# Kernel optimization log

Hardware: AMD Instinct MI355X
Metric: run time of the kernel (lower is better)

Reference implementation:

```python
import jax, jax.numpy as jnp
import numpy as np

MAX_SEQ, D, VOCAB, N_LAYERS = 2048, 256, 240, 6
DH = 64.0  # scale used inside RelativeGlobalAttention
BATCH = 4


def _pos_embedding():
    # sin(pow(pos*1e-5, i/D) - pi/2 * ((i+1)%2)), exactly as in __init__
    pos = np.arange(MAX_SEQ, dtype=np.float64)[:, None]
    i = np.arange(D, dtype=np.float64)[None, :]
    ang = np.power(pos * 1e-5, i / D) - np.pi * 0.5 * ((i + 1) % 2)
    return jnp.asarray(np.sin(ang), dtype=jnp.float32)  # [L, D]


def _skew(QE):
    # pad a zero column in front, reshape [B,L,L+1]->[B,L+1,L], drop first row
    B, L, _ = QE.shape
    cat = jnp.concatenate([jnp.zeros((B, L, 1), QE.dtype), QE], axis=2)
    return cat.reshape(B, L + 1, L)[:, 1:, :]


def _rel_attn(x, Wq, Wk, Wv):
    Q = x @ Wq  # [B,L,D]
    K = x @ Wk
    V = x @ Wv
    QE = jnp.einsum('bld,bmd->blm', Q, K - Q)      # Q @ (K-Q)^T
    Srel = _skew(QE)
    QKt = jnp.einsum('bld,bmd->blm', Q, K)
    scores = (QKt + Srel) / jnp.sqrt(jnp.asarray(DH, x.dtype))
    probs = jax.nn.softmax(scores, axis=-1)        # no causal mask in source
    return probs @ V


def setup_inputs() -> dict:
    key = jax.random.key(0)
    ks = jax.random.split(key, 16)
    s = 1.0 / np.sqrt(D)
    mk = lambda k, shape, sc: (jax.random.normal(k, shape, jnp.float32) * sc)
    inp = {
        'tokens': jax.random.randint(ks[0], (BATCH, MAX_SEQ), 0, VOCAB),
        'embed_table': mk(ks[1], (VOCAB, D), 0.05),
        'Wq1': mk(ks[2], (N_LAYERS, D, D), s),
        'Wk1': mk(ks[3], (N_LAYERS, D, D), s),
        'Wv1': mk(ks[4], (N_LAYERS, D, D), s),
        'Wq2': mk(ks[5], (N_LAYERS, D, D), s),
        'Wk2': mk(ks[6], (N_LAYERS, D, D), s),
        'Wv2': mk(ks[7], (N_LAYERS, D, D), s),
        'Wf1': mk(ks[8], (N_LAYERS, D, D), s),
        'bf1': jnp.zeros((N_LAYERS, D), jnp.float32),
        'Wf2': mk(ks[9], (N_LAYERS, D, D), s),
        'bf2': jnp.zeros((N_LAYERS, D), jnp.float32),
        'Wfc': mk(ks[10], (MAX_SEQ * D, VOCAB), 1.0 / np.sqrt(MAX_SEQ * D)),
        'bfc': jnp.zeros((VOCAB,), jnp.float32),
    }
    return inp


def reference(tokens, embed_table, Wq1, Wk1, Wv1, Wq2, Wk2, Wv2,
              Wf1, bf1, Wf2, bf2, Wfc, bfc):
    x = embed_table[tokens] + _pos_embedding()[None]  # [B,L,D]
    for i in range(N_LAYERS):
        x = _rel_attn(x, Wq1[i], Wk1[i], Wv1[i]) + x
        x = _rel_attn(x, Wq2[i], Wk2[i], Wv2[i]) + x
        h = jax.nn.leaky_relu(x @ Wf1[i] + bf1[i], negative_slope=0.2)
        x = h @ Wf2[i] + bf2[i]
        # NOTE: BatchNorm layers exist in source but are never called in _decoder
    flat = x.reshape(x.shape[0], -1)  # [B, L*D]
    return jax.nn.softmax(flat @ Wfc + bfc, axis=-1)  # [B, vocab]
```

## Files before the change

### kernel.cpp

```cpp
#include <hip/hip_runtime.h>
#include <hip/hip_fp16.h>

typedef unsigned short u16;
typedef unsigned int   u32;

#define BB 4
#define LL 2048
#define DD 256
#define VV 240
#define NLAYERS 6

static constexpr long BLD = (long)BB * LL * DD;
static constexpr long LD_ = (long)LL * DD;
static constexpr long LxL = (long)LL * LL;
static constexpr long BLL = (long)BB * LxL;

typedef _Float16 h8  __attribute__((ext_vector_type(8)));
typedef float  f32x4 __attribute__((ext_vector_type(4)));

__device__ __forceinline__ u16 f2h(float f) {
    _Float16 h = (_Float16)f;
    return __builtin_bit_cast(u16, h);
}
__device__ __forceinline__ float h2f(u16 u) {
    return (float)__builtin_bit_cast(_Float16, u);
}

__device__ __forceinline__ void gl16(const void* g, void* l) {
    __builtin_amdgcn_global_load_lds((const __attribute__((address_space(1))) void*)g,
                                     (__attribute__((address_space(3))) void*)l, 16, 0, 0);
}

__global__ __launch_bounds__(256)
void embed_kernel(const int* __restrict__ tokens, const float* __restrict__ table,
                  float* __restrict__ x, u16* __restrict__ xh)
{
    long idx = (long)blockIdx.x * 256 + threadIdx.x;
    if (idx >= BLD) return;
    int i  = (int)(idx & (DD - 1));
    long bl = idx >> 8;
    int l  = (int)(bl & (LL - 1));
    int tok = tokens[bl];
    float base = (float)l * 1e-5f;
    float p = powf(base, (float)i * (1.0f / (float)DD));
    float ang = p - ((i & 1) ? 0.0f : 1.57079632679489662f);
    float v = table[(long)tok * DD + i] + sinf(ang);
    x[idx] = v;
    xh[idx] = f2h(v);
}

template<bool DIFF>
__global__ __launch_bounds__(256)
void wconv(const float* __restrict__ W, const float* __restrict__ Wsub,
           u16* __restrict__ Wt, long lstride)
{
    int blk = blockIdx.x;
    int m  = blk >> 6;
    int ti = (blk >> 3) & 7;
    int tj = blk & 7;
    const float* src = W + (long)m * 65536;
    u16* dst = Wt + (long)m * lstride;
    __shared__ float tile[32][33];
    int t = threadIdx.x;
    int c = t & 31, r8 = t >> 5;
    #pragma unroll
    for (int p = 0; p < 4; ++p) {
        int r = r8 + p * 8;
        long off = (long)(ti * 32 + r) * 256 + tj * 32 + c;
        float v = src[off];
        if constexpr (DIFF) v -= Wsub[(long)m * 65536 + off];
        tile[r][c] = v;
    }
    __syncthreads();
    #pragma unroll
    for (int p = 0; p < 4; ++p) {
        int n = r8 + p * 8;
        dst[(long)(tj * 32 + n) * 256 + ti * 32 + c] = f2h(tile[c][n]);
    }
}

template<int EPI, int BM, int BN>
__global__ __launch_bounds__(256)
void gemm_mfma(const u16* __restrict__ A, const u16* __restrict__ B,
               const u16* __restrict__ B2,
               const float* __restrict__ bias, const float* __restrict__ Cres,
               float* __restrict__ Cf, u16* __restrict__ Ch,
               u16* __restrict__ Ch2, u16* __restrict__ Ch3, u16* __restrict__ Ch4,
               int M, int N, int K, int ldA,
               long sA, long sB, long sC)
{
    constexpr int FM = BM / 32, FN = BN / 32;
    __shared__ u16 As[2][BM * 32];
    __shared__ u16 Bs[2][BN * 32];
    const int bz = blockIdx.z;
    A += (long)bz * sA;
    const int bm = blockIdx.y * BM;
    const int bn = blockIdx.x * BN;
    int bnb = bn;
    const u16* Bp;
    if constexpr (EPI & 128) {
        Bp = (bn >= LL) ? B2 : B;
        if (bn >= LL) bnb = bn - LL;
        Bp += (long)bz * sB;
    } else {
        Bp = B + (long)bz * sB;
    }
    if constexpr (EPI & 4)  Cres += (long)bz * sC;
    if constexpr (EPI & 8)  Cf   += (long)bz * sC;
    if constexpr ((EPI & 16) && !(EPI & (64 | 128))) Ch += (long)bz * sC;

    const int t = threadIdx.x;
    const int lane = t & 63, wave = t >> 6;
    const int wm = (wave >> 1) * (BM / 2), wn = (wave & 1) * (BN / 2);

    f32x4 acc[FM][FN];
    #pragma unroll
    for (int i = 0; i < FM; ++i)
        #pragma unroll
        for (int j = 0; j < FN; ++j)
            acc[i][j] = (f32x4){0.f, 0.f, 0.f, 0.f};

    const u16* gA0 = A  + (long)(bm  + (t >> 2)) * ldA + (t & 3) * 8;
    const u16* gB0 = Bp + (long)(bnb + (t >> 2)) * K   + (t & 3) * 8;

    const int arow = wm + (lane & 15);
    const int brow = wn + (lane & 15);
    const int ko = (lane >> 4) * 8;

    #define STAGE(buf, koff) do {                                              \
        gl16(gA0 + (koff), &As[buf][wave * 512]);                              \
        if constexpr (BM == 128) gl16(gA0 + 64L * ldA + (koff),                \
                                      &As[buf][2048 + wave * 512]);            \
        gl16(gB0 + (koff), &Bs[buf][wave * 512]);                              \
        if constexpr (BN == 128) gl16(gB0 + 64L * K + (koff),                  \
                                      &Bs[buf][2048 + wave * 512]);            \
    } while (0)

    STAGE(0, 0);
    int cur = 0;
    for (int k0 = 0; k0 < K; k0 += 32) {
        __syncthreads();
        if (k0 + 32 < K) {
            if (cur) STAGE(0, k0 + 32);
            else     STAGE(1, k0 + 32);
        }
        h8 af[FM], bf[FN];
        #pragma unroll
        for (int i = 0; i < FM; ++i) af[i] = *(const h8*)&As[cur][(arow + i * 16) * 32 + ko];
        #pragma unroll
        for (int j = 0; j < FN; ++j) bf[j] = *(const h8*)&Bs[cur][(brow + j * 16) * 32 + ko];
        #pragma unroll
        for (int i = 0; i < FM; ++i)
            #pragma unroll
            for (int j = 0; j < FN; ++j)
                acc[i][j] = __builtin_amdgcn_mfma_f32_16x16x32_f16(af[i], bf[j], acc[i][j], 0, 0, 0);
        cur ^= 1;
    }
    #undef STAGE

    const int colc = lane & 15;
    const int rowb = (lane >> 4) * 4;
    if constexpr (EPI & 64) {
        const int seg = bn >> 8;
        const int nb  = bn & 255;
        if (seg < 3) {
            u16* dst = (seg == 0) ? Ch : ((seg == 1) ? Ch2 : Ch3);
            #pragma unroll
            for (int i = 0; i < FM; ++i)
                #pragma unroll
                for (int j = 0; j < FN; ++j) {
                    int nn = nb + wn + j * 16 + colc;
                    #pragma unroll
                    for (int r = 0; r < 4; ++r) {
                        long row = bm + wm + i * 16 + rowb + r;
                        dst[row * DD + nn] = f2h(acc[i][j][r]);
                    }
                }
        } else {
            #pragma unroll
            for (int i = 0; i < FM; ++i) {
                int r0 = bm + wm + i * 16 + rowb;
                int b  = r0 >> 11;
                int m0 = r0 & (LL - 1);
                #pragma unroll
                for (int j = 0; j < FN; ++j) {
                    int nn = nb + wn + j * 16 + colc;
                    f32x4 v = acc[i][j];
                    ushort4 pk;
                    pk.x = f2h(v.x); pk.y = f2h(v.y); pk.z = f2h(v.z); pk.w = f2h(v.w);
                    *(ushort4*)&Ch4[((long)b * DD + nn) * LL + m0] = pk;
                }
            }
        }
    } else if constexpr (EPI & 128) {
        u16* dst = ((bn >= LL) ? Ch2 : Ch) + (long)bz * sC;
        const int nb = bn & (LL - 1);
        #pragma unroll
        for (int i = 0; i < FM; ++i)
            #pragma unroll
            for (int j = 0; j < FN; ++j) {
                int n = nb + wn + j * 16 + colc;
                #pragma unroll
                for (int r = 0; r < 4; ++r) {
                    long row = bm + wm + i * 16 + rowb + r;
                    dst[row * LL + n] = f2h(acc[i][j][r]);
                }
            }
    } else {
        #pragma unroll
        for (int i = 0; i < FM; ++i) {
            #pragma unroll
            for (int j = 0; j < FN; ++j) {
                int n = bn + wn + j * 16 + colc;
                float bv = (EPI & 1) ? bias[n] : 0.f;
                #pragma unroll
                for (int r = 0; r < 4; ++r) {
                    long row = bm + wm + i * 16 + rowb + r;
                    float val = acc[i][j][r] + bv;
                    if (EPI & 2) val = (val >= 0.f) ? val : 0.2f * val;
                    long off = row * (long)N + n;
                    if (EPI & 4) val += Cres[off];
                    if (EPI & 8) Cf[off] = val;
                    if (EPI & 16) Ch[off] = f2h(val);
                }
            }
        }
    }
}

__global__ __launch_bounds__(256)
void skew_softmax(u16* __restrict__ S1, const u16* __restrict__ QE)
{
    const int bi = blockIdx.x;
    const int b = bi >> 11;
    const int i = bi & (LL - 1);
    u16* srow = S1 + (long)bi * LL;
    const u16* qe_i  = QE + ((long)b * LL + i) * LL;
    const u16* qe_i1 = qe_i + ((i + 1 < LL) ? LL : 0);
    const int t = threadIdx.x;

    uint4 sv = ((const uint4*)srow)[t];
    const u16* se = (const u16*)&sv;
    float vals[8];
    float mx = -1e30f;
    #pragma unroll
    for (int j = 0; j < 8; ++j) {
        int m = t * 8 + j;
        float srel;
        if (m <= i)            srel = h2f(qe_i[m - i + (LL - 1)]);
        else if (m == i + 1)   srel = 0.f;
        else                   srel = h2f(qe_i1[m - i - 2]);
        float s = (h2f(se[j]) + srel) * 0.125f;
        vals[j] = s;
        mx = fmaxf(mx, s);
    }
    #pragma unroll
    for (int off = 32; off >= 1; off >>= 1)
        mx = fmaxf(mx, __shfl_xor(mx, off, 64));
    __shared__ float redm[4], reds[4];
    const int wid = t >> 6;
    if ((t & 63) == 0) redm[wid] = mx;
    __syncthreads();
    mx = fmaxf(fmaxf(redm[0], redm[1]), fmaxf(redm[2], redm[3]));

    float sum = 0.f;
    #pragma unroll
    for (int j = 0; j < 8; ++j) { vals[j] = expf(vals[j] - mx); sum += vals[j]; }
    #pragma unroll
    for (int off = 32; off >= 1; off >>= 1)
        sum += __shfl_xor(sum, off, 64);
    if ((t & 63) == 0) reds[wid] = sum;
    __syncthreads();
    sum = reds[0] + reds[1] + reds[2] + reds[3];
    float inv = 1.0f / sum;
    uint4 ov;
    u16* oe = (u16*)&ov;
    #pragma unroll
    for (int j = 0; j < 8; ++j) oe[j] = f2h(vals[j] * inv);
    ((uint4*)srow)[t] = ov;
}

__global__ __launch_bounds__(960)
void fc_partial(const float* __restrict__ x, const float* __restrict__ W,
                float* __restrict__ part)
{
    const int v = threadIdx.x;
    const int b = threadIdx.y;
    const int chunk = blockIdx.x;
    const int KC = (int)(LD_ / 256);
    const long k0 = (long)chunk * KC;
    const float* xb = x + (long)b * LD_ + k0;
    const float* Wp = W + k0 * VV + v;
    float acc = 0.f;
    #pragma unroll 4
    for (int k2 = 0; k2 < KC; ++k2)
        acc = fmaf(xb[k2], Wp[(long)k2 * VV], acc);
    part[((long)chunk * BB + b) * VV + v] = acc;
}

__global__ __launch_bounds__(960)
void fc_finish(const float* __restrict__ part, const float* __restrict__ bias,
               float* __restrict__ out)
{
    const int v = threadIdx.x, b = threadIdx.y;
    float acc = bias[v];
    for (int c = 0; c < 256; ++c)
        acc += part[((long)c * BB + b) * VV + v];
    __shared__ float lds[BB][VV];
    __shared__ float mxs[BB], sms[BB];
    lds[b][v] = acc;
    __syncthreads();
    if (v == 0) {
        float m = -1e30f;
        for (int j = 0; j < VV; ++j) m = fmaxf(m, lds[b][j]);
        float s = 0.f;
        for (int j = 0; j < VV; ++j) s += expf(lds[b][j] - m);
        mxs[b] = m; sms[b] = s;
    }
    __syncthreads();
    out[b * VV + v] = expf(lds[b][v] - mxs[b]) / sms[b];
}

extern "C" void kernel_launch(void* const* d_in, const int* in_sizes, int n_in,
                              void* d_out, int out_size, void* d_ws, size_t ws_size,
                              hipStream_t stream)
{
    const int*   tokens = (const int*)d_in[0];
    const float* table  = (const float*)d_in[1];
    const float* Wq1 = (const float*)d_in[2];
    const float* Wk1 = (const float*)d_in[3];
    const float* Wv1 = (const float*)d_in[4];
    const float* Wq2 = (const float*)d_in[5];
    const float* Wk2 = (const float*)d_in[6];
    const float* Wv2 = (const float*)d_in[7];
    const float* Wf1 = (const float*)d_in[8];
    const float* bf1 = (const float*)d_in[9];
    const float* Wf2 = (const float*)d_in[10];
    const float* bf2 = (const float*)d_in[11];
    const float* Wfc = (const float*)d_in[12];
    const float* bfc = (const float*)d_in[13];

    char* p = (char*)d_ws;
    float* x  = (float*)p; p += BLD * 4;
    u16* xh = (u16*)p;     p += BLD * 2;
    u16* qb = (u16*)p;     p += BLD * 2;
    u16* kb = (u16*)p;     p += BLD * 2;
    u16* eb = (u16*)p;     p += BLD * 2;
    u16* vt = (u16*)p;     p += BLD * 2;
    u16* S1 = (u16*)p;     p += BLL * 2;
    u16* QE = (u16*)p;     p += BLL * 2;
    u16* qkevw = (u16*)p;  p += 12L * 4 * 65536 * 2;
    u16* fw = (u16*)p;     p += 12L * 65536 * 2;
    float* part = (float*)p;
    u16* hb = qb;

    const long LS = 4 * 65536;
    wconv<false><<<384, 256, 0, stream>>>(Wq1, nullptr, qkevw + 0L * 65536, LS);
    wconv<false><<<384, 256, 0, stream>>>(Wk1, nullptr, qkevw + 1L * 65536, LS);
    wconv<true ><<<384, 256, 0, stream>>>(Wk1, Wq1,     qkevw + 2L * 65536, LS);
    wconv<false><<<384, 256, 0, stream>>>(Wv1, nullptr, qkevw + 3L * 65536, LS);
    wconv<false><<<384, 256, 0, stream>>>(Wq2, nullptr, qkevw + 24L * 65536, LS);
    wconv<true ><<<384, 256, 0, stream>>>(Wk2, Wq2,     qkevw + 24L * 65536 + 2 * 65536, LS);
    wconv<false><<<384, 256, 0, stream>>>(Wk2, nullptr, qkevw + 24L * 65536 + 1 * 65536, LS);
    wconv<false><<<384, 256, 0, stream>>>(Wv2, nullptr, qkevw + 24L * 65536 + 3 * 65536, LS);
    wconv<false><<<384, 256, 0, stream>>>(Wf1, nullptr, fw, 65536);
    wconv<false><<<384, 256, 0, stream>>>(Wf2, nullptr, fw + 6L * 65536, 65536);

    embed_kernel<<<(int)((BLD + 255) / 256), 256, 0, stream>>>(tokens, table, x, xh);

    const dim3 gqkev(8, 64, 1);
    const dim3 gscore(32, 16, BB);
    const dim3 gpv(4, 32, BB);
    const dim3 gffn(4, 128, 1);

    for (int layer = 0; layer < NLAYERS; ++layer) {
        for (int half = 0; half < 2; ++half) {
            const u16* wqkev = qkevw + ((long)(half * 6 + layer)) * LS;
            gemm_mfma<64, 128, 128><<<gqkev, 256, 0, stream>>>(
                xh, wqkev, nullptr, nullptr, nullptr, nullptr, qb, kb, eb, vt,
                BB * LL, 1024, DD, DD, 0, 0, 0);
            gemm_mfma<128, 128, 128><<<gscore, 256, 0, stream>>>(
                qb, kb, eb, nullptr, nullptr, nullptr, S1, QE, nullptr, nullptr,
                LL, LL, DD, DD, LD_, LD_, LxL);
            skew_softmax<<<BB * LL, 256, 0, stream>>>(S1, QE);
            gemm_mfma<4 | 8 | 16, 64, 64><<<gpv, 256, 0, stream>>>(
                S1, vt, nullptr, nullptr, x, x, xh, nullptr, nullptr, nullptr,
                LL, DD, LL, LL, LxL, LD_, LD_);
        }
        gemm_mfma<1 | 2 | 16, 64, 64><<<gffn, 256, 0, stream>>>(
            xh, fw + (long)layer * 65536, nullptr, bf1 + layer * DD, nullptr,
            nullptr, hb, nullptr, nullptr, nullptr, BB * LL, DD, DD, DD, 0, 0, 0);
        gemm_mfma<1 | 8 | 16, 64, 64><<<gffn, 256, 0, stream>>>(
            hb, fw + (long)(6 + layer) * 65536, nullptr, bf2 + layer * DD, nullptr,
            x, xh, nullptr, nullptr, nullptr, BB * LL, DD, DD, DD, 0, 0, 0);
    }

    fc_partial<<<256, dim3(VV, BB, 1), 0, stream>>>(x, Wfc, part);
    fc_finish<<<1, dim3(VV, BB, 1), 0, stream>>>(part, bfc, (float*)d_out);
}
```

Before: 1.783 ms.

## Fuse skew-softmax with PV GEMM using online softmax

Replaces the separate skew+softmax kernel and the P@V GEMM with one kernel that streams S1/QE tiles, computes the skewed scores with an online (flash-style) softmax, and multiplies by V tiles staged in LDS via MFMA. This removes the write-back and re-read of the normalized probability matrix. In exchange, each 32-row block handles all 256 output columns over the full sequence, giving only 256 blocks with heavy LDS use and a sync per 64-column tile, which may limit occupancy and latency hiding.

```diff
diff --git a/kernel.cpp b/kernel.cpp
--- a/kernel.cpp
+++ b/kernel.cpp
@@ -229,55 +229,141 @@
 }
 
 __global__ __launch_bounds__(256)
-void skew_softmax(u16* __restrict__ S1, const u16* __restrict__ QE)
-{
-    const int bi = blockIdx.x;
-    const int b = bi >> 11;
-    const int i = bi & (LL - 1);
-    u16* srow = S1 + (long)bi * LL;
-    const u16* qe_i  = QE + ((long)b * LL + i) * LL;
+void attn_fused(const u16* __restrict__ S1, const u16* __restrict__ QE,
+                const u16* __restrict__ vt, float* __restrict__ x,
+                u16* __restrict__ xh)
+{
+    __shared__ u16 Vs[256 * 64];
+    __shared__ u16 Ps[32 * 72];
+    __shared__ float scLds[32], lLds[32];
+
+    const int b  = blockIdx.z;
+    const int i0 = blockIdx.x * 32;
+    const int t  = threadIdx.x;
+    const int lane = t & 63, wave = t >> 6;
+    const int r  = t >> 3;
+    const int sl = t & 7;
+    const int i  = i0 + r;
+
+    const u16* s1row = S1 + (long)b * LxL + (long)i * LL;
+    const u16* qe_i  = QE + (long)b * LxL + (long)i * LL;
     const u16* qe_i1 = qe_i + ((i + 1 < LL) ? LL : 0);
-    const int t = threadIdx.x;
-
-    uint4 sv = ((const uint4*)srow)[t];
-    const u16* se = (const u16*)&sv;
-    float vals[8];
-    float mx = -1e30f;
+    const u16* vb    = vt + (long)b * LD_;
+
+    const int colc = lane & 15;
+    const int rowb = (lane >> 4) * 4;
+    const int wn   = wave * 64;
+
+    f32x4 acc[2][4];
     #pragma unroll
-    for (int j = 0; j < 8; ++j) {
-        int m = t * 8 + j;
-        float srel;
-        if (m <= i)            srel = h2f(qe_i[m - i + (LL - 1)]);
-        else if (m == i + 1)   srel = 0.f;
-        else                   srel = h2f(qe_i1[m - i - 2]);
-        float s = (h2f(se[j]) + srel) * 0.125f;
-        vals[j] = s;
-        mx = fmaxf(mx, s);
-    }
+    for (int rf = 0; rf < 2; ++rf)
+        #pragma unroll
+        for (int cf = 0; cf < 4; ++cf)
+            acc[rf][cf] = (f32x4){0.f, 0.f, 0.f, 0.f};
+
+    float row_m = -1e30f, row_l = 0.f;
+
+    #define STAGEV(m0) do {                                                     \
+        _Pragma("unroll")                                                       \
+        for (int u = 0; u < 8; ++u) {                                           \
+            int c = t + u * 256;                                                \
+            int d = c >> 3;                                                     \
+            int s2 = (c & 7) ^ (d & 7);                                         \
+            gl16(vb + (long)d * LL + (m0) + s2 * 8, &Vs[c * 8]);                \
+        }                                                                       \
+    } while (0)
+
+    STAGEV(0);
+    for (int mt = 0; mt < 32; ++mt) {
+        const int m0 = mt * 64;
+        uint4 sv = *(const uint4*)&s1row[m0 + sl * 8];
+        const u16* se = (const u16*)&sv;
+        float s[8];
+        float pmax = -1e30f;
+        #pragma unroll
+        for (int j = 0; j < 8; ++j) {
+            int m = m0 + sl * 8 + j;
+            float srel;
+            if (m <= i)           srel = h2f(qe_i[m - i + (LL - 1)]);
+            else if (m == i + 1)  srel = 0.f;
+            else                  srel = h2f(qe_i1[m - i - 2]);
+            s[j] = (h2f(se[j]) + srel) * 0.125f;
+            pmax = fmaxf(pmax, s[j]);
+        }
+        pmax = fmaxf(pmax, __shfl_xor(pmax, 1));
+        pmax = fmaxf(pmax, __shfl_xor(pmax, 2));
+        pmax = fmaxf(pmax, __shfl_xor(pmax, 4));
+        float newm  = fmaxf(row_m, pmax);
+        float scale = __expf(row_m - newm);
+        row_m = newm;
+        union { uint4 v4; u16 h[8]; } P;
+        float psum = 0.f;
+        #pragma unroll
+        for (int j = 0; j < 8; ++j) {
+            float e = __expf(s[j] - newm);
+            psum += e;
+            P.h[j] = f2h(e);
+        }
+        psum += __shfl_xor(psum, 1);
+        psum += __shfl_xor(psum, 2);
+        psum += __shfl_xor(psum, 4);
+        row_l = row_l * scale + psum;
+        *(uint4*)&Ps[r * 72 + sl * 8] = P.v4;
+        if (sl == 0) scLds[r] = scale;
+        __syncthreads();
+
+        #pragma unroll
+        for (int rf = 0; rf < 2; ++rf) {
+            float c0 = scLds[rf * 16 + rowb + 0];
+            float c1 = scLds[rf * 16 + rowb + 1];
+            float c2 = scLds[rf * 16 + rowb + 2];
+            float c3 = scLds[rf * 16 + rowb + 3];
+            #pragma unroll
+            for (int cf = 0; cf < 4; ++cf) {
+                acc[rf][cf][0] *= c0; acc[rf][cf][1] *= c1;
+                acc[rf][cf][2] *= c2; acc[rf][cf][3] *= c3;
+            }
+        }
+        #pragma unroll
+        for (int ks = 0; ks < 2; ++ks) {
+            h8 pa[2];
+            #pragma unroll
+            for (int rf = 0; rf < 2; ++rf)
+                pa[rf] = *(const h8*)&Ps[(rf * 16 + colc) * 72 + (ks * 4 + (lane >> 4)) * 8];
+            #pragma unroll
+            for (int cf = 0; cf < 4; ++cf) {
+                int d  = wn + cf * 16 + colc;
+                int sg = ks * 4 + (lane >> 4);
+                h8 bv = *(const h8*)&Vs[(d * 8 + (sg ^ (d & 7))) * 8];
+                #pragma unroll
+                for (int rf = 0; rf < 2; ++rf)
+                    acc[rf][cf] = __builtin_amdgcn_mfma_f32_16x16x32_f16(pa[rf], bv, acc[rf][cf], 0, 0, 0);
+            }
+        }
+        __syncthreads();
+        if (mt < 31) STAGEV(m0 + 64);
+    }
+    #undef STAGEV
+
+    if (sl == 0) lLds[r] = row_l;
+    __syncthreads();
+
     #pragma unroll
-    for (int off = 32; off >= 1; off >>= 1)
-        mx = fmaxf(mx, __shfl_xor(mx, off, 64));
-    __shared__ float redm[4], reds[4];
-    const int wid = t >> 6;
-    if ((t & 63) == 0) redm[wid] = mx;
-    __syncthreads();
-    mx = fmaxf(fmaxf(redm[0], redm[1]), fmaxf(redm[2], redm[3]));
-
-    float sum = 0.f;
-    #pragma unroll
-    for (int j = 0; j < 8; ++j) { vals[j] = expf(vals[j] - mx); sum += vals[j]; }
-    #pragma unroll
-    for (int off = 32; off >= 1; off >>= 1)
-        sum += __shfl_xor(sum, off, 64);
-    if ((t & 63) == 0) reds[wid] = sum;
-    __syncthreads();
-    sum = reds[0] + reds[1] + reds[2] + reds[3];
-    float inv = 1.0f / sum;
-    uint4 ov;
-    u16* oe = (u16*)&ov;
-    #pragma unroll
-    for (int j = 0; j < 8; ++j) oe[j] = f2h(vals[j] * inv);
-    ((uint4*)srow)[t] = ov;
+    for (int rf = 0; rf < 2; ++rf) {
+        #pragma unroll
+        for (int rr = 0; rr < 4; ++rr) {
+            int row = rf * 16 + rowb + rr;
+            float inv = 1.0f / lLds[row];
+            #pragma unroll
+            for (int cf = 0; cf < 4; ++cf) {
+                int col = wn + cf * 16 + colc;
+                long off = (long)b * LD_ + (long)(i0 + row) * DD + col;
+                float val = acc[rf][cf][rr] * inv + x[off];
+                x[off]  = val;
+                xh[off] = f2h(val);
+            }
+        }
+    }
 }
 
 __global__ __launch_bounds__(960)
@@ -370,7 +456,7 @@
 
     const dim3 gqkev(8, 64, 1);
     const dim3 gscore(32, 16, BB);
-    const dim3 gpv(4, 32, BB);
+    const dim3 gattn(LL / 32, 1, BB);
     const dim3 gffn(4, 128, 1);
 
     for (int layer = 0; layer < NLAYERS; ++layer) {
@@ -382,10 +468,7 @@
             gemm_mfma<128, 128, 128><<<gscore, 256, 0, stream>>>(
                 qb, kb, eb, nullptr, nullptr, nullptr, S1, QE, nullptr, nullptr,
                 LL, LL, DD, DD, LD_, LD_, LxL);
-            skew_softmax<<<BB * LL, 256, 0, stream>>>(S1, QE);
-            gemm_mfma<4 | 8 | 16, 64, 64><<<gpv, 256, 0, stream>>>(
-                S1, vt, nullptr, nullptr, x, x, xh, nullptr, nullptr, nullptr,
-                LL, DD, LL, LL, LxL, LD_, LD_);
+            attn_fused<<<gattn, 256, 0, stream>>>(S1, QE, vt, x, xh);
         }
         gemm_mfma<1 | 2 | 16, 64, 64><<<gffn, 256, 0, stream>>>(
             xh, fw + (long)layer * 65536, nullptr, bf1 + layer * DD, nullptr,
```

After: 2.232 ms. +25.2%, slower.
